# Kernel tuning notes

Measured on AMD Instinct MI355X. Metric: run time of the kernel, lower is better.

Reference implementation:

```python
import jax, jax.numpy as jnp
import numpy as np

TEMP = float(np.e)

def _normalize(v):
    n = jnp.linalg.norm(v, axis=-1, keepdims=True)
    return v / jnp.maximum(n, 1e-12)

def setup_inputs() -> dict:
    key = jax.random.key(0)
    ks = jax.random.split(key, 18)
    N, D, H, O, E = 8192, 1024, 2048, 1024, 8
    s = 0.02
    return {
        "x": jax.random.normal(ks[0], (N, D), jnp.float32),
        "gate_w": jax.random.normal(ks[1], (D, E), jnp.float32) * s,
        "gate_b": jnp.zeros((E,), jnp.float32),
        "ph_w1": jax.random.normal(ks[2], (D, 32), jnp.float32) * s,
        "ph_b1": jnp.zeros((32,), jnp.float32),
        "ph_w2": jax.random.normal(ks[3], (32, 16), jnp.float32) * s,
        "ph_b2": jnp.zeros((16,), jnp.float32),
        "cl_w1": jax.random.normal(ks[4], (D, 16), jnp.float32) * s,
        "cl_b1": jnp.zeros((16,), jnp.float32),
        "cl_w2": jax.random.normal(ks[5], (16, 1), jnp.float32) * s,
        "cl_b2": jnp.zeros((1,), jnp.float32),
        "sigs": jax.random.normal(ks[6], (E, 16), jnp.float32) * 0.1,
        "e_w1": jax.random.normal(ks[7], (E, D, H), jnp.float32) * s,
        "e_b1": jnp.zeros((E, H), jnp.float32),
        "e_w2": jax.random.normal(ks[8], (E, H, O), jnp.float32) * s,
        "e_b2": jnp.zeros((E, O), jnp.float32),
    }

def reference(x, gate_w, gate_b, ph_w1, ph_b1, ph_w2, ph_b2,
              cl_w1, cl_b1, cl_w2, cl_b2, sigs, e_w1, e_b1, e_w2, e_b2):
    E = sigs.shape[0]
    # gating
    scores = (x @ gate_w + gate_b) / TEMP            # [N, E]
    probs = jax.nn.softmax(scores, axis=-1)
    # ph signature matching
    ph_feat = _normalize(jax.nn.relu(x @ ph_w1 + ph_b1) @ ph_w2 + ph_b2)  # [N, 16]
    sig_n = _normalize(sigs)                          # [E, 16]
    ph_match = (ph_feat @ sig_n.T + 1.0) / 2.0        # [N, E]
    effective = probs * ph_match
    # data-dependent k (torch uses .item(); here traced int used only in mask compare)
    clarity = jax.nn.sigmoid(jax.nn.relu(x @ cl_w1 + cl_b1) @ cl_w2 + cl_b2)  # [N,1]
    n_active = E - clarity[:, 0] * (E - 2)
    k = jnp.clip(jnp.floor(n_active.mean() + 0.5).astype(jnp.int32), 2, E)
    # rank-based top-k mask (jit-compatible for traced k)
    ranks = jnp.argsort(jnp.argsort(-effective, axis=-1), axis=-1)  # [N, E]
    mask = (ranks < k).astype(effective.dtype)
    weights = effective * mask
    weights = weights / (weights.sum(axis=-1, keepdims=True) + 1e-8)
    # load-balance loss
    f = (weights > 0).astype(probs.dtype).mean(axis=0)
    P = probs.mean(axis=0)
    lb_loss = 0.01 * E * (f * P).sum()
    # dense all-expert MLP (dropout is identity at eval)
    h = jax.nn.relu(jnp.einsum('nd,edh->neh', x, e_w1) + e_b1)   # [N, E, H]
    outs = jnp.einsum('neh,eho->neo', h, e_w2) + e_b2            # [N, E, O]
    y = jnp.einsum('ne,neo->no', weights, outs)                   # [N, O]
    return y, lb_loss
```

## Files before the change

kernel.cpp:

```cpp
#include <hip/hip_runtime.h>
#include <hip/hip_bf16.h>
#include <stdint.h>

typedef __attribute__((ext_vector_type(8))) _Float16 half8;
typedef __attribute__((ext_vector_type(4))) float f32x4;
typedef __attribute__((ext_vector_type(4))) unsigned short us4;
typedef __attribute__((ext_vector_type(8))) unsigned short us8;

#define N_TOK 8192
#define DIM   1024
#define HDIM  2048
#define ODIM  1024

__device__ __forceinline__ unsigned short f2h(float f) {
  _Float16 h = (_Float16)f;
  union { _Float16 h; unsigned short u; } c; c.h = h; return c.u;
}

__device__ __forceinline__ void gload_lds16(const void* g, void* l) {
  __builtin_amdgcn_global_load_lds(
      (const __attribute__((address_space(1))) unsigned int*)g,
      (__attribute__((address_space(3))) unsigned int*)l, 16, 0, 0);
}

template <int EPI>
__global__ __launch_bounds__(256) void gemm_kernel(
    const unsigned short* __restrict__ A, const unsigned short* __restrict__ B,
    int M, int N, int K,
    const float* __restrict__ bias, unsigned short* __restrict__ Hout,
    const float* __restrict__ Wg, int e, float* __restrict__ Y)
{
  __shared__ half8 ldsA[2][512];
  __shared__ half8 ldsB[2][512];
  const int lane = threadIdx.x & 63, wid = threadIdx.x >> 6;
  const int wr = wid >> 1, wc = wid & 1;

  const int nwg = gridDim.x * gridDim.y;
  const int orig = blockIdx.y * gridDim.x + blockIdx.x;
  const int qq = nwg >> 3;
  const int swz = (orig & 7) * qq + (orig >> 3);
  const int bx = swz % gridDim.x, by = swz / gridDim.x;
  const int rowbase = by * 128, colbase = bx * 128;

  f32x4 acc[4][4];
#pragma unroll
  for (int m = 0; m < 4; ++m)
#pragma unroll
    for (int n = 0; n < 4; ++n) acc[m][n] = f32x4{0.f, 0.f, 0.f, 0.f};

  auto stage = [&](int buf, int ktile) {
#pragma unroll
    for (int i = 0; i < 4; ++i) {
      const int c = wid * 4 + i;
      const int cc = c & 7, kq = cc >> 1, half = cc & 1;
      const int koff = ktile * 32 + kq * 8;
      if (c < 8)
        gload_lds16(A + (size_t)(rowbase + half * 64 + lane) * K + koff,
                    &ldsA[buf][kq * 128 + half * 64]);
      else
        gload_lds16(B + (size_t)(colbase + half * 64 + lane) * K + koff,
                    &ldsB[buf][kq * 128 + half * 64]);
    }
  };

  const int KT = K >> 5;
  stage(0, 0);
  for (int kt = 0; kt < KT; ++kt) {
    const int buf = kt & 1;
    __syncthreads();
    if (kt + 1 < KT) stage(buf ^ 1, kt + 1);

    half8 af[4], bfr[4];
    const int kqo = (lane >> 4) * 128;
    const int rA = wr * 64 + (lane & 15);
    const int rB = wc * 64 + (lane & 15);
#pragma unroll
    for (int m = 0; m < 4; ++m) af[m] = ldsA[buf][kqo + rA + m * 16];
#pragma unroll
    for (int n = 0; n < 4; ++n) bfr[n] = ldsB[buf][kqo + rB + n * 16];
#pragma unroll
    for (int m = 0; m < 4; ++m)
#pragma unroll
      for (int n = 0; n < 4; ++n)
        acc[m][n] = __builtin_amdgcn_mfma_f32_16x16x32_f16(af[m], bfr[n], acc[m][n], 0, 0, 0);
  }

  const int r0 = rowbase + wr * 64, c0 = colbase + wc * 64;
  if (EPI == 1) {
#pragma unroll
    for (int n = 0; n < 4; ++n) {
      const int col = c0 + n * 16 + (lane & 15);
      const float bv = bias[col];
#pragma unroll
      for (int m = 0; m < 4; ++m)
#pragma unroll
        for (int r = 0; r < 4; ++r) {
          const int row = r0 + m * 16 + (lane >> 4) * 4 + r;
          float v = acc[m][n][r] + bv;
          v = v > 0.f ? v : 0.f;
          Hout[(size_t)row * N + col] = f2h(v);
        }
    }
  } else {
#pragma unroll
    for (int m = 0; m < 4; ++m)
#pragma unroll
      for (int r = 0; r < 4; ++r) {
        const int row = r0 + m * 16 + (lane >> 4) * 4 + r;
        const float wv = Wg[row * 8 + e];
#pragma unroll
        for (int n = 0; n < 4; ++n) {
          const int col = c0 + n * 16 + (lane & 15);
          const size_t idx = (size_t)row * N + col;
          Y[idx] += wv * acc[m][n][r];
        }
      }
  }
}

__global__ __launch_bounds__(256) void gating_kernel(
    const float* __restrict__ x,
    const float* __restrict__ gate_w, const float* __restrict__ gate_b,
    const float* __restrict__ ph_w1, const float* __restrict__ ph_b1,
    const float* __restrict__ ph_w2, const float* __restrict__ ph_b2,
    const float* __restrict__ cl_w1, const float* __restrict__ cl_b1,
    const float* __restrict__ cl_w2, const float* __restrict__ cl_b2,
    const float* __restrict__ sigs,
    unsigned short* __restrict__ xh,
    float* __restrict__ eff_o,
    float* __restrict__ pclar, float* __restrict__ pP)
{
  const int lane = threadIdx.x & 63, wid = threadIdx.x >> 6;
  const int tok = blockIdx.x * 4 + wid;

  float g[8], p1[32], c1[16];
#pragma unroll
  for (int i = 0; i < 8; ++i) g[i] = 0.f;
#pragma unroll
  for (int i = 0; i < 32; ++i) p1[i] = 0.f;
#pragma unroll
  for (int i = 0; i < 16; ++i) c1[i] = 0.f;

  const f32x4* x4 = (const f32x4*)(x + (size_t)tok * DIM);
  us4* xh4 = (us4*)(xh + (size_t)tok * DIM);
#pragma unroll
  for (int d0 = 0; d0 < 4; ++d0) {
    const f32x4 xv = x4[d0 * 64 + lane];
    us4 ov;
#pragma unroll
    for (int j = 0; j < 4; ++j) {
      const int d = (d0 * 64 + lane) * 4 + j;
      const float xd = xv[j];
      ov[j] = f2h(xd);
      const f32x4* gw = (const f32x4*)(gate_w + d * 8);
#pragma unroll
      for (int q = 0; q < 2; ++q) { const f32x4 w = gw[q];
#pragma unroll
        for (int r = 0; r < 4; ++r) g[q * 4 + r] += xd * w[r]; }
      const f32x4* pw = (const f32x4*)(ph_w1 + d * 32);
#pragma unroll
      for (int q = 0; q < 8; ++q) { const f32x4 w = pw[q];
#pragma unroll
        for (int r = 0; r < 4; ++r) p1[q * 4 + r] += xd * w[r]; }
      const f32x4* cw = (const f32x4*)(cl_w1 + d * 16);
#pragma unroll
      for (int q = 0; q < 4; ++q) { const f32x4 w = cw[q];
#pragma unroll
        for (int r = 0; r < 4; ++r) c1[q * 4 + r] += xd * w[r]; }
    }
    xh4[d0 * 64 + lane] = ov;
  }
#pragma unroll
  for (int i = 0; i < 8; ++i)
#pragma unroll
    for (int s = 0; s < 6; ++s) g[i] += __shfl_xor(g[i], 1 << s);
#pragma unroll
  for (int i = 0; i < 32; ++i)
#pragma unroll
    for (int s = 0; s < 6; ++s) p1[i] += __shfl_xor(p1[i], 1 << s);
#pragma unroll
  for (int i = 0; i < 16; ++i)
#pragma unroll
    for (int s = 0; s < 6; ++s) c1[i] += __shfl_xor(c1[i], 1 << s);

  float sc[8]; float mx = -1e30f;
#pragma unroll
  for (int k = 0; k < 8; ++k) { sc[k] = (g[k] + gate_b[k]) / 2.718281828459045f; mx = fmaxf(mx, sc[k]); }
  float ex[8]; float sum = 0.f;
#pragma unroll
  for (int k = 0; k < 8; ++k) { ex[k] = expf(sc[k] - mx); sum += ex[k]; }
  float pe[8];
#pragma unroll
  for (int k = 0; k < 8; ++k) pe[k] = ex[k] / sum;

  float rh[32];
#pragma unroll
  for (int h = 0; h < 32; ++h) { const float v = p1[h] + ph_b1[h]; rh[h] = v > 0.f ? v : 0.f; }
  float feat[16];
#pragma unroll
  for (int q = 0; q < 16; ++q) {
    float f = ph_b2[q];
#pragma unroll
    for (int h = 0; h < 32; ++h) f += rh[h] * ph_w2[h * 16 + q];
    feat[q] = f;
  }
  float nn = 0.f;
#pragma unroll
  for (int q = 0; q < 16; ++q) nn += feat[q] * feat[q];
  const float den = fmaxf(sqrtf(nn), 1e-12f);
#pragma unroll
  for (int q = 0; q < 16; ++q) feat[q] = feat[q] / den;

  float eff[8];
#pragma unroll
  for (int k = 0; k < 8; ++k) {
    float s2 = 0.f;
#pragma unroll
    for (int q = 0; q < 16; ++q) { const float sv = sigs[k * 16 + q]; s2 += sv * sv; }
    const float sden = fmaxf(sqrtf(s2), 1e-12f);
    float dot = 0.f;
#pragma unroll
    for (int q = 0; q < 16; ++q) dot += feat[q] * (sigs[k * 16 + q] / sden);
    eff[k] = pe[k] * ((dot + 1.0f) / 2.0f);
  }

  float z = cl_b2[0];
#pragma unroll
  for (int c = 0; c < 16; ++c) { float v = c1[c] + cl_b1[c]; v = v > 0.f ? v : 0.f; z += v * cl_w2[c]; }
  const float clar = 1.0f / (1.0f + expf(-z));

  if (lane == 0) {
#pragma unroll
    for (int k = 0; k < 8; ++k) eff_o[tok * 8 + k] = eff[k];
  }
  __shared__ float shc[4];
  __shared__ float shP[4][8];
  if (lane == 0) { shc[wid] = clar;
#pragma unroll
    for (int k = 0; k < 8; ++k) shP[wid][k] = pe[k]; }
  __syncthreads();
  if (threadIdx.x == 0) {
    pclar[blockIdx.x] = shc[0] + shc[1] + shc[2] + shc[3];
#pragma unroll
    for (int k = 0; k < 8; ++k)
      pP[blockIdx.x * 8 + k] = shP[0][k] + shP[1][k] + shP[2][k] + shP[3][k];
  }
}

__global__ __launch_bounds__(256) void weights_kernel(
    const float* __restrict__ eff_i, const float* __restrict__ pclar,
    float* __restrict__ wout, int* __restrict__ f_part)
{
  __shared__ float red[256];
  __shared__ int cnt[8];
  __shared__ int ksh;
  const int tid = threadIdx.x;
  float s = 0.f;
  for (int i = tid; i < 2048; i += 256) s += pclar[i];
  red[tid] = s; __syncthreads();
  for (int off = 128; off > 0; off >>= 1) { if (tid < off) red[tid] += red[tid + off]; __syncthreads(); }
  if (tid == 0) {
    const float mean_na = 8.0f - 6.0f * (red[0] / 8192.0f);
    int k = (int)floorf(mean_na + 0.5f);
    ksh = k < 2 ? 2 : (k > 8 ? 8 : k);
  }
  if (tid < 8) cnt[tid] = 0;
  __syncthreads();
  const int k = ksh;
  const int t = blockIdx.x * 256 + tid;
  const f32x4* ep = (const f32x4*)(eff_i + t * 8);
  const f32x4 ea = ep[0], eb = ep[1];
  const float ef[8] = {ea[0], ea[1], ea[2], ea[3], eb[0], eb[1], eb[2], eb[3]};
  float w[8]; float wsum = 0.f; int act[8];
#pragma unroll
  for (int e2 = 0; e2 < 8; ++e2) {
    int r = 0;
#pragma unroll
    for (int j = 0; j < 8; ++j) r += (int)((ef[j] > ef[e2]) || ((j < e2) && (ef[j] == ef[e2])));
    const float we = (r < k) ? ef[e2] : 0.f;
    w[e2] = we; wsum += we; act[e2] = we > 0.f ? 1 : 0;
  }
  const float dn = wsum + 1e-8f;
#pragma unroll
  for (int e2 = 0; e2 < 8; ++e2) wout[t * 8 + e2] = w[e2] / dn;
#pragma unroll
  for (int e2 = 0; e2 < 8; ++e2) if (act[e2]) atomicAdd(&cnt[e2], 1);
  __syncthreads();
  if (tid < 8) f_part[blockIdx.x * 8 + tid] = cnt[tid];
}

__global__ __launch_bounds__(256) void lb_kernel(
    const float* __restrict__ pP, const int* __restrict__ f_part, float* __restrict__ lbout)
{
  __shared__ float red[256];
  __shared__ float Ps[8], Fs[8];
  const int tid = threadIdx.x;
  for (int e2 = 0; e2 < 8; ++e2) {
    float s = 0.f;
    for (int i = tid; i < 2048; i += 256) s += pP[i * 8 + e2];
    red[tid] = s; __syncthreads();
    for (int off = 128; off > 0; off >>= 1) { if (tid < off) red[tid] += red[tid + off]; __syncthreads(); }
    if (tid == 0) Ps[e2] = red[0];
    __syncthreads();
    red[tid] = (tid < 32) ? (float)f_part[tid * 8 + e2] : 0.f;
    __syncthreads();
    for (int off = 128; off > 0; off >>= 1) { if (tid < off) red[tid] += red[tid + off]; __syncthreads(); }
    if (tid == 0) Fs[e2] = red[0];
    __syncthreads();
  }
  if (tid == 0) {
    float lb = 0.f;
    for (int e2 = 0; e2 < 8; ++e2) lb += (Fs[e2] / 8192.0f) * (Ps[e2] / 8192.0f);
    lbout[0] = 0.01f * 8.0f * lb;
  }
}

__global__ __launch_bounds__(256) void yinit_kernel(
    const float* __restrict__ w, const float* __restrict__ b2, float* __restrict__ y)
{
  const int idx = blockIdx.x * 256 + threadIdx.x;
  const int n = idx >> 8, o4 = idx & 255;
  const f32x4* bv = (const f32x4*)b2;
  f32x4 a = f32x4{0.f, 0.f, 0.f, 0.f};
  const float* wr = w + n * 8;
#pragma unroll
  for (int e2 = 0; e2 < 8; ++e2) a += wr[e2] * bv[e2 * 256 + o4];
  ((f32x4*)y)[idx] = a;
}

__global__ __launch_bounds__(256) void transpose_kernel(
    const float* __restrict__ in, unsigned short* __restrict__ out, int R, int C)
{
  __shared__ __align__(16) unsigned short t[64][72];
  const float* ip = in + (size_t)blockIdx.z * R * C;
  unsigned short* op = out + (size_t)blockIdx.z * R * C;
  const int r0 = blockIdx.y * 64, c0 = blockIdx.x * 64;
  const int tr = threadIdx.x >> 4, tc4 = (threadIdx.x & 15) * 4;
#pragma unroll
  for (int i = 0; i < 4; ++i) {
    const int rr = tr + i * 16;
    const f32x4 v = *(const f32x4*)(ip + (size_t)(r0 + rr) * C + c0 + tc4);
#pragma unroll
    for (int j = 0; j < 4; ++j) t[tc4 + j][rr] = f2h(v[j]);
  }
  __syncthreads();
  const int oc = threadIdx.x >> 3, or8 = (threadIdx.x & 7) * 8;
#pragma unroll
  for (int i = 0; i < 2; ++i) {
    const int c = oc + i * 32;
    const us8 v = *(const us8*)&t[c][or8];
    *(us8*)(op + (size_t)(c0 + c) * R + r0 + or8) = v;
  }
}

extern "C" void kernel_launch(void* const* d_in, const int* in_sizes, int n_in,
                              void* d_out, int out_size, void* d_ws, size_t ws_size,
                              hipStream_t stream)
{
  const float* x      = (const float*)d_in[0];
  const float* gate_w = (const float*)d_in[1];
  const float* gate_b = (const float*)d_in[2];
  const float* ph_w1  = (const float*)d_in[3];
  const float* ph_b1  = (const float*)d_in[4];
  const float* ph_w2  = (const float*)d_in[5];
  const float* ph_b2  = (const float*)d_in[6];
  const float* cl_w1  = (const float*)d_in[7];
  const float* cl_b1  = (const float*)d_in[8];
  const float* cl_w2  = (const float*)d_in[9];
  const float* cl_b2  = (const float*)d_in[10];
  const float* sigs   = (const float*)d_in[11];
  const float* e_w1   = (const float*)d_in[12];
  const float* e_b1   = (const float*)d_in[13];
  const float* e_w2   = (const float*)d_in[14];
  const float* e_b2   = (const float*)d_in[15];
  float* y = (float*)d_out;
  char* ws = (char*)d_ws;

  float* eff    = (float*)(ws + 262144);
  float* wts    = (float*)(ws + 524288);
  float* pclar  = (float*)(ws + 786432);
  float* pP     = (float*)(ws + 794624);
  int*   f_part = (int*)(ws + 860160);
  unsigned short* xh  = (unsigned short*)(ws + 1048576);
  unsigned short* W1T = (unsigned short*)(ws + 17825792u);
  unsigned short* W2T = (unsigned short*)(ws + 51380224u);
  unsigned short* Hh  = (unsigned short*)(ws + 84934656u);

  transpose_kernel<<<dim3(32, 16, 8), 256, 0, stream>>>(e_w1, W1T, 1024, 2048);
  transpose_kernel<<<dim3(16, 32, 8), 256, 0, stream>>>(e_w2, W2T, 2048, 1024);
  gating_kernel<<<2048, 256, 0, stream>>>(x, gate_w, gate_b, ph_w1, ph_b1, ph_w2, ph_b2,
                                          cl_w1, cl_b1, cl_w2, cl_b2, sigs,
                                          xh, eff, pclar, pP);
  weights_kernel<<<32, 256, 0, stream>>>(eff, pclar, wts, f_part);
  lb_kernel<<<1, 256, 0, stream>>>(pP, f_part, y + (size_t)8192 * 1024);
  yinit_kernel<<<8192, 256, 0, stream>>>(wts, e_b2, y);

  for (int e2 = 0; e2 < 8; ++e2) {
    gemm_kernel<1><<<dim3(16, 64), 256, 0, stream>>>(
        xh, W1T + (size_t)e2 * HDIM * DIM, N_TOK, HDIM, DIM,
        e_b1 + e2 * HDIM, Hh, nullptr, 0, nullptr);
    gemm_kernel<2><<<dim3(8, 64), 256, 0, stream>>>(
        Hh, W2T + (size_t)e2 * ODIM * HDIM, N_TOK, ODIM, HDIM,
        nullptr, nullptr, wts, e2, y);
  }
}
```

Baseline: 1.918 ms.

## Route only active tokens through each expert via gathered token lists

```diff
diff --git a/kernel.cpp b/kernel.cpp
--- a/kernel.cpp
+++ b/kernel.cpp
@@ -6,6 +6,7 @@
 typedef __attribute__((ext_vector_type(4))) float f32x4;
 typedef __attribute__((ext_vector_type(4))) unsigned short us4;
 typedef __attribute__((ext_vector_type(8))) unsigned short us8;
+typedef __attribute__((ext_vector_type(4))) int i32x4;
 
 #define N_TOK 8192
 #define DIM   1024
@@ -26,9 +27,11 @@
 template <int EPI>
 __global__ __launch_bounds__(256) void gemm_kernel(
     const unsigned short* __restrict__ A, const unsigned short* __restrict__ B,
-    int M, int N, int K,
+    int N, int K,
     const float* __restrict__ bias, unsigned short* __restrict__ Hout,
-    const float* __restrict__ Wg, int e, float* __restrict__ Y)
+    const float* __restrict__ Wg, int e, float* __restrict__ Y,
+    const int* __restrict__ lst, const int* __restrict__ cntTrue,
+    const int* __restrict__ cntPad)
 {
   __shared__ half8 ldsA[2][512];
   __shared__ half8 ldsB[2][512];
@@ -42,6 +45,12 @@
   const int bx = swz % gridDim.x, by = swz / gridDim.x;
   const int rowbase = by * 128, colbase = bx * 128;
 
+  const int padc = cntPad[e];
+  if (rowbase >= padc) return;
+
+  int rG0 = rowbase + lane, rG1 = rowbase + 64 + lane;
+  if (EPI == 1) { rG0 = lst[rG0]; rG1 = lst[rG1]; }
+
   f32x4 acc[4][4];
 #pragma unroll
   for (int m = 0; m < 4; ++m)
@@ -54,12 +63,14 @@
       const int c = wid * 4 + i;
       const int cc = c & 7, kq = cc >> 1, half = cc & 1;
       const int koff = ktile * 32 + kq * 8;
-      if (c < 8)
-        gload_lds16(A + (size_t)(rowbase + half * 64 + lane) * K + koff,
+      if (c < 8) {
+        const int arow = half ? rG1 : rG0;
+        gload_lds16(A + (size_t)arow * K + koff,
                     &ldsA[buf][kq * 128 + half * 64]);
-      else
+      } else {
         gload_lds16(B + (size_t)(colbase + half * 64 + lane) * K + koff,
                     &ldsB[buf][kq * 128 + half * 64]);
+      }
     }
   };
 
@@ -95,26 +106,32 @@
       for (int m = 0; m < 4; ++m)
 #pragma unroll
         for (int r = 0; r < 4; ++r) {
-          const int row = r0 + m * 16 + (lane >> 4) * 4 + r;
+          const int slot = r0 + m * 16 + (lane >> 4) * 4 + r;
           float v = acc[m][n][r] + bv;
           v = v > 0.f ? v : 0.f;
-          Hout[(size_t)row * N + col] = f2h(v);
+          Hout[(size_t)slot * N + col] = f2h(v);
         }
     }
   } else {
-#pragma unroll
-    for (int m = 0; m < 4; ++m)
+    const int cntT = cntTrue[e];
+#pragma unroll
+    for (int m = 0; m < 4; ++m) {
+      const int sbase = r0 + m * 16 + (lane >> 4) * 4;
+      const i32x4 og = *(const i32x4*)&lst[sbase];
 #pragma unroll
       for (int r = 0; r < 4; ++r) {
-        const int row = r0 + m * 16 + (lane >> 4) * 4 + r;
-        const float wv = Wg[row * 8 + e];
-#pragma unroll
-        for (int n = 0; n < 4; ++n) {
-          const int col = c0 + n * 16 + (lane & 15);
-          const size_t idx = (size_t)row * N + col;
-          Y[idx] += wv * acc[m][n][r];
+        const int slot = sbase + r;
+        if (slot < cntT) {
+          const int otok = og[r];
+          const float wv = Wg[otok * 8 + e];
+#pragma unroll
+          for (int n = 0; n < 4; ++n) {
+            const int col = c0 + n * 16 + (lane & 15);
+            Y[(size_t)otok * ODIM + col] += wv * acc[m][n][r];
+          }
         }
       }
+    }
   }
 }
 
@@ -247,9 +264,14 @@
   }
 }
 
+__global__ void zero_kernel(int* __restrict__ gcount) {
+  if (threadIdx.x < 8) gcount[threadIdx.x] = 0;
+}
+
 __global__ __launch_bounds__(256) void weights_kernel(
     const float* __restrict__ eff_i, const float* __restrict__ pclar,
-    float* __restrict__ wout, int* __restrict__ f_part)
+    float* __restrict__ wout, int* __restrict__ f_part,
+    int* __restrict__ gcount, int* __restrict__ lst)
 {
   __shared__ float red[256];
   __shared__ int cnt[8];
@@ -284,9 +306,29 @@
 #pragma unroll
   for (int e2 = 0; e2 < 8; ++e2) wout[t * 8 + e2] = w[e2] / dn;
 #pragma unroll
-  for (int e2 = 0; e2 < 8; ++e2) if (act[e2]) atomicAdd(&cnt[e2], 1);
+  for (int e2 = 0; e2 < 8; ++e2)
+    if (act[e2]) {
+      atomicAdd(&cnt[e2], 1);
+      const int p = atomicAdd(&gcount[e2], 1);
+      lst[e2 * N_TOK + p] = t;
+    }
   __syncthreads();
   if (tid < 8) f_part[blockIdx.x * 8 + tid] = cnt[tid];
+}
+
+__global__ __launch_bounds__(256) void pad_kernel(
+    const int* __restrict__ gcount, int* __restrict__ gpad, int* __restrict__ lst)
+{
+  const int tid = threadIdx.x;
+  for (int e2 = 0; e2 < 8; ++e2) {
+    const int a = gcount[e2];
+    const int pc = (a + 127) & ~127;
+    if (tid == 0) gpad[e2] = pc;
+    if (a > 0) {
+      const int last = lst[e2 * N_TOK + a - 1];
+      for (int i = a + tid; i < pc; i += 256) lst[e2 * N_TOK + i] = last;
+    }
+  }
 }
 
 __global__ __launch_bounds__(256) void lb_kernel(
@@ -331,7 +373,7 @@
 __global__ __launch_bounds__(256) void transpose_kernel(
     const float* __restrict__ in, unsigned short* __restrict__ out, int R, int C)
 {
-  __shared__ __align__(16) unsigned short t[64][72];
+  __shared__ __align__(16) unsigned short tb[64][72];
   const float* ip = in + (size_t)blockIdx.z * R * C;
   unsigned short* op = out + (size_t)blockIdx.z * R * C;
   const int r0 = blockIdx.y * 64, c0 = blockIdx.x * 64;
@@ -341,14 +383,14 @@
     const int rr = tr + i * 16;
     const f32x4 v = *(const f32x4*)(ip + (size_t)(r0 + rr) * C + c0 + tc4);
 #pragma unroll
-    for (int j = 0; j < 4; ++j) t[tc4 + j][rr] = f2h(v[j]);
+    for (int j = 0; j < 4; ++j) tb[tc4 + j][rr] = f2h(v[j]);
   }
   __syncthreads();
   const int oc = threadIdx.x >> 3, or8 = (threadIdx.x & 7) * 8;
 #pragma unroll
   for (int i = 0; i < 2; ++i) {
     const int c = oc + i * 32;
-    const us8 v = *(const us8*)&t[c][or8];
+    const us8 v = *(const us8*)&tb[c][or8];
     *(us8*)(op + (size_t)(c0 + c) * R + r0 + or8) = v;
   }
 }
@@ -376,11 +418,14 @@
   float* y = (float*)d_out;
   char* ws = (char*)d_ws;
 
-  float* eff    = (float*)(ws + 262144);
-  float* wts    = (float*)(ws + 524288);
-  float* pclar  = (float*)(ws + 786432);
-  float* pP     = (float*)(ws + 794624);
-  int*   f_part = (int*)(ws + 860160);
+  float* eff    = (float*)(ws + 0);
+  float* wts    = (float*)(ws + 262144);
+  float* pclar  = (float*)(ws + 524288);
+  float* pP     = (float*)(ws + 532480);
+  int*   f_part = (int*)(ws + 598016);
+  int*   gcount = (int*)(ws + 599040);
+  int*   gpad   = (int*)(ws + 599072);
+  int*   lst    = (int*)(ws + 655360);
   unsigned short* xh  = (unsigned short*)(ws + 1048576);
   unsigned short* W1T = (unsigned short*)(ws + 17825792u);
   unsigned short* W2T = (unsigned short*)(ws + 51380224u);
@@ -391,16 +436,20 @@
   gating_kernel<<<2048, 256, 0, stream>>>(x, gate_w, gate_b, ph_w1, ph_b1, ph_w2, ph_b2,
                                           cl_w1, cl_b1, cl_w2, cl_b2, sigs,
                                           xh, eff, pclar, pP);
-  weights_kernel<<<32, 256, 0, stream>>>(eff, pclar, wts, f_part);
-  lb_kernel<<<1, 256, 0, stream>>>(pP, f_part, y + (size_t)8192 * 1024);
+  zero_kernel<<<1, 64, 0, stream>>>(gcount);
+  weights_kernel<<<32, 256, 0, stream>>>(eff, pclar, wts, f_part, gcount, lst);
+  pad_kernel<<<1, 256, 0, stream>>>(gcount, gpad, lst);
+  lb_kernel<<<1, 256, 0, stream>>>(pP, f_part, y + (size_t)N_TOK * ODIM);
   yinit_kernel<<<8192, 256, 0, stream>>>(wts, e_b2, y);
 
   for (int e2 = 0; e2 < 8; ++e2) {
     gemm_kernel<1><<<dim3(16, 64), 256, 0, stream>>>(
-        xh, W1T + (size_t)e2 * HDIM * DIM, N_TOK, HDIM, DIM,
-        e_b1 + e2 * HDIM, Hh, nullptr, 0, nullptr);
+        xh, W1T + (size_t)e2 * HDIM * DIM, HDIM, DIM,
+        e_b1 + e2 * HDIM, Hh, nullptr, e2, nullptr,
+        lst + (size_t)e2 * N_TOK, gcount, gpad);
     gemm_kernel<2><<<dim3(8, 64), 256, 0, stream>>>(
-        Hh, W2T + (size_t)e2 * ODIM * HDIM, N_TOK, ODIM, HDIM,
-        nullptr, nullptr, wts, e2, y);
-  }
-}
+        Hh, W2T + (size_t)e2 * ODIM * HDIM, ODIM, HDIM,
+        nullptr, nullptr, wts, e2, y,
+        lst + (size_t)e2 * N_TOK, gcount, gpad);
+  }
+}
```

Result: slower. 1.977 ms (+3.1%).
